# Optimization experiments

Hardware: AMD Instinct MI355X
Metric: run time of the kernel (lower is better)

## Reference

```python
import jax, jax.numpy as jnp
import numpy as np
import math

D_MODEL, N_HEADS, D_HEAD, D_MLP = 768, 12, 64, 3072
LN_EPS = 1e-5
INIT_STD = 0.02


def gelu_new(x):
    # GPT-2 'new' gelu: 0.5*x*(1+tanh(sqrt(2/pi)*(x+0.044715*x^3)))
    c = math.sqrt(2.0 / math.pi)
    return 0.5 * x * (1.0 + jnp.tanh(c * (x + 0.044715 * jnp.power(x, 3.0))))


def layer_norm(x, w, b):
    mu = jnp.mean(x, axis=-1, keepdims=True)
    xc = x - mu
    scale = jnp.sqrt(jnp.mean(xc * xc, axis=-1, keepdims=True) + LN_EPS)
    return (xc / scale) * w + b


def setup_inputs() -> dict:
    key = jax.random.key(0)
    ks = jax.random.split(key, 8)
    resid_pre = jax.random.normal(ks[0], (8, 1024, D_MODEL), dtype=jnp.float32)
    W_Q = jax.random.normal(ks[1], (N_HEADS, D_MODEL, D_HEAD), dtype=jnp.float32) * INIT_STD
    W_K = jax.random.normal(ks[2], (N_HEADS, D_MODEL, D_HEAD), dtype=jnp.float32) * INIT_STD
    W_V = jax.random.normal(ks[3], (N_HEADS, D_MODEL, D_HEAD), dtype=jnp.float32) * INIT_STD
    W_O = jax.random.normal(ks[4], (N_HEADS, D_HEAD, D_MODEL), dtype=jnp.float32) * INIT_STD
    W_in = jax.random.normal(ks[5], (D_MODEL, D_MLP), dtype=jnp.float32) * INIT_STD
    W_out = jax.random.normal(ks[6], (D_MLP, D_MODEL), dtype=jnp.float32) * INIT_STD
    return {
        'resid_pre': resid_pre,
        'ln1_w': jnp.ones((D_MODEL,), jnp.float32), 'ln1_b': jnp.zeros((D_MODEL,), jnp.float32),
        'W_Q': W_Q, 'b_Q': jnp.zeros((N_HEADS, D_HEAD), jnp.float32),
        'W_K': W_K, 'b_K': jnp.zeros((N_HEADS, D_HEAD), jnp.float32),
        'W_V': W_V, 'b_V': jnp.zeros((N_HEADS, D_HEAD), jnp.float32),
        'W_O': W_O, 'b_O': jnp.zeros((D_MODEL,), jnp.float32),
        'ln2_w': jnp.ones((D_MODEL,), jnp.float32), 'ln2_b': jnp.zeros((D_MODEL,), jnp.float32),
        'W_in': W_in, 'b_in': jnp.zeros((D_MLP,), jnp.float32),
        'W_out': W_out, 'b_out': jnp.zeros((D_MODEL,), jnp.float32),
    }


def attention(x, W_Q, b_Q, W_K, b_K, W_V, b_V, W_O, b_O):
    # x: [b, s, d_model]
    q = jnp.einsum('bsd,hde->bshe', x, W_Q) + b_Q
    k = jnp.einsum('bsd,hde->bshe', x, W_K) + b_K
    v = jnp.einsum('bsd,hde->bshe', x, W_V) + b_V
    scores = jnp.einsum('bqhe,bkhe->bhqk', q, k) / math.sqrt(D_HEAD)
    s = x.shape[1]
    causal = jnp.triu(jnp.ones((s, s), dtype=bool), k=1)
    scores = jnp.where(causal, -jnp.inf, scores)
    pattern = jax.nn.softmax(scores, axis=-1)
    pattern = jnp.where(jnp.isnan(pattern), 0.0, pattern)
    z = jnp.einsum('bhqk,bkhe->bqhe', pattern, v)
    # per-head projection then sum over heads; b_O/n_heads per head sums to b_O
    return jnp.einsum('bqhe,hed->bqd', z, W_O) + b_O


def reference(resid_pre, ln1_w, ln1_b, W_Q, b_Q, W_K, b_K, W_V, b_V, W_O, b_O,
              ln2_w, ln2_b, W_in, b_in, W_out, b_out):
    normed1 = layer_norm(resid_pre, ln1_w, ln1_b)
    attn_out = attention(normed1, W_Q, b_Q, W_K, b_K, W_V, b_V, W_O, b_O)
    residual = resid_pre + attn_out
    normed2 = layer_norm(residual, ln2_w, ln2_b)
    pre = jnp.einsum('bsd,dm->bsm', normed2, W_in) + b_in
    mlp_out = jnp.einsum('bsm,md->bsd', gelu_new(pre), W_out) + b_out
    return residual + mlp_out
```

## Files before the change

kernel.cpp:

```cpp
#include <hip/hip_runtime.h>
#include <hip/hip_bf16.h>
#include <stdint.h>
#include <math.h>

typedef __bf16 bf16x8 __attribute__((ext_vector_type(8)));
typedef float f32x4 __attribute__((ext_vector_type(4)));
using bf16 = __hip_bfloat16;

__device__ inline float bf2f(bf16 x) { return __bfloat162float(x); }
__device__ inline bf16 f2bf(float x) { return __float2bfloat16(x); }

__device__ inline f32x4 mfma16(bf16x8 a, bf16x8 b, f32x4 c) {
  return __builtin_amdgcn_mfma_f32_16x16x32_bf16(a, b, c, 0, 0, 0);
}

__device__ inline void async16(const bf16* g, bf16* l) {
  __builtin_amdgcn_global_load_lds(
      (const __attribute__((address_space(1))) unsigned int*)g,
      (__attribute__((address_space(3))) unsigned int*)l, 16, 0, 0);
}

__device__ inline float gelu_new(float x) {
  float u2 = 1.5957691216057308f * (x + 0.044715f * x * x * x);
  float e = __expf(u2);
  float t = 1.0f - 2.0f * __builtin_amdgcn_rcpf(e + 1.0f);
  return 0.5f * x * (1.0f + t);
}

__device__ inline void ln_body(const float* __restrict__ x, const float* __restrict__ w,
                               const float* __restrict__ bb, bf16* __restrict__ out,
                               int row, int t, float* red) {
  size_t base = (size_t)row * 768;
  float v0 = x[base + t];
  float v1 = x[base + t + 256];
  float v2 = x[base + t + 512];
  float s = v0 + v1 + v2;
  float ss = v0 * v0 + v1 * v1 + v2 * v2;
#pragma unroll
  for (int off = 32; off > 0; off >>= 1) {
    s += __shfl_down(s, off, 64);
    ss += __shfl_down(ss, off, 64);
  }
  int wv = t >> 6, ln = t & 63;
  if (ln == 0) { red[wv] = s; red[4 + wv] = ss; }
  __syncthreads();
  s = red[0] + red[1] + red[2] + red[3];
  ss = red[4] + red[5] + red[6] + red[7];
  float mu = s * (1.0f / 768.0f);
  float var = ss * (1.0f / 768.0f) - mu * mu;
  float rinv = rsqrtf(var + 1e-5f);
  out[base + t]       = f2bf((v0 - mu) * rinv * w[t]       + bb[t]);
  out[base + t + 256] = f2bf((v1 - mu) * rinv * w[t + 256] + bb[t + 256]);
  out[base + t + 512] = f2bf((v2 - mu) * rinv * w[t + 512] + bb[t + 512]);
}

__global__ __launch_bounds__(256) void ln_kernel(const float* __restrict__ x,
                                                 const float* __restrict__ w,
                                                 const float* __restrict__ bb,
                                                 bf16* __restrict__ out) {
  __shared__ float red[8];
  ln_body(x, w, bb, out, blockIdx.x, threadIdx.x, red);
}

__device__ inline void transpose_body(const float* __restrict__ in, bf16* __restrict__ out,
                                      int R, int C, int bx, int by, int t,
                                      float (*tile)[33]) {
  int tx = t & 31, ty = t >> 5;
  int r0 = bx * 32, c0 = by * 32;
#pragma unroll
  for (int j = 0; j < 32; j += 8)
    tile[ty + j][tx] = in[(size_t)(r0 + ty + j) * C + c0 + tx];
  __syncthreads();
#pragma unroll
  for (int j = 0; j < 32; j += 8)
    out[(size_t)(c0 + ty + j) * R + r0 + tx] = f2bf(tile[tx][ty + j]);
}

__global__ __launch_bounds__(256) void prep_all(
    const float* __restrict__ resid_pre, const float* __restrict__ ln1_w,
    const float* __restrict__ ln1_b, bf16* __restrict__ n1,
    const float* __restrict__ Wq, const float* __restrict__ Wk,
    const float* __restrict__ Wv, bf16* __restrict__ Wqkv_t,
    const float* __restrict__ W_O, bf16* __restrict__ Wo_t,
    const float* __restrict__ W_in, bf16* __restrict__ Win_t,
    const float* __restrict__ W_out, bf16* __restrict__ Wout_t,
    const float* __restrict__ bq, const float* __restrict__ bk,
    const float* __restrict__ bv, float* __restrict__ bias_qkv) {
  __shared__ float tile[32][33];
  const int t = threadIdx.x;
  int bid = blockIdx.x;
  if (bid < 8192) {
    ln_body(resid_pre, ln1_w, ln1_b, n1, bid, t, &tile[0][0]);
    return;
  }
  bid -= 8192;
  if (bid < 1728) {
    int z = bid / 48, r = bid - z * 48;
    int which = z / 12, h = z - which * 12;
    const float* W = (which == 0) ? Wq : ((which == 1) ? Wk : Wv);
    transpose_body(W + (size_t)h * 768 * 64,
                   Wqkv_t + (size_t)which * 589824 + (size_t)h * 64 * 768,
                   768, 64, r % 24, r / 24, t, tile);
    return;
  }
  bid -= 1728;
  if (bid < 576) {
    transpose_body(W_O, Wo_t, 768, 768, bid % 24, bid / 24, t, tile);
    return;
  }
  bid -= 576;
  if (bid < 2304) {
    transpose_body(W_in, Win_t, 768, 3072, bid % 24, bid / 24, t, tile);
    return;
  }
  bid -= 2304;
  if (bid < 2304) {
    transpose_body(W_out, Wout_t, 3072, 768, bid % 96, bid / 96, t, tile);
    return;
  }
  bid -= 2304;
  int i = bid * 256 + t;
  if (i < 2304)
    bias_qkv[i] = (i < 768) ? bq[i] : ((i < 1536) ? bk[i - 768] : bv[i - 1536]);
}

enum { MODE_QKV = 0, MODE_ADDF = 2, MODE_GELU = 3 };

template <int MODE, int MROWS>
__global__ __launch_bounds__(256) void gemm_bt(
    const bf16* __restrict__ A, const bf16* __restrict__ BT,
    const float* __restrict__ bias,
    const float* __restrict__ addend,
    float* __restrict__ out_f32,
    bf16* __restrict__ out_bf16,
    int M, int N, int K) {
  constexpr int MI = MROWS / 32;
  __shared__ __align__(16) bf16 smem[(MROWS + 128) * 64];
  bf16* Alds = smem;
  bf16* Blds = smem + MROWS * 64;
  const int t = threadIdx.x;
  const int wave = t >> 6, lane = t & 63;
  const int lm = lane & 15, quad = lane >> 4;
  const int wm = wave >> 1, wn = wave & 1;
  const int m0 = blockIdx.x * MROWS, n0 = blockIdx.y * 128;

  f32x4 acc[MI][4] = {};

  for (int k0 = 0; k0 < K; k0 += 64) {
#pragma unroll
    for (int i = 0; i < MI; i++) {
      int c = i * 256 + t;
      int r = c >> 3, cs = c & 7;
      async16(A + (size_t)(m0 + r) * K + k0 + ((cs ^ (r & 7)) << 3), &Alds[c * 8]);
    }
#pragma unroll
    for (int i = 0; i < 4; i++) {
      int c = i * 256 + t;
      int r = c >> 3, cs = c & 7;
      async16(BT + (size_t)(n0 + r) * K + k0 + ((cs ^ (r & 7)) << 3), &Blds[c * 8]);
    }
    __syncthreads();
#pragma unroll
    for (int kk = 0; kk < 64; kk += 32) {
      const int cbase = kk >> 3;
      bf16x8 af[MI], bfr[4];
#pragma unroll
      for (int mi = 0; mi < MI; mi++)
        af[mi] = *(const bf16x8*)&Alds[(wm * (MROWS / 2) + mi * 16 + lm) * 64 +
                                       (((cbase + quad) ^ (lm & 7)) << 3)];
#pragma unroll
      for (int ni = 0; ni < 4; ni++)
        bfr[ni] = *(const bf16x8*)&Blds[(wn * 64 + ni * 16 + lm) * 64 +
                                        (((cbase + quad) ^ (lm & 7)) << 3)];
#pragma unroll
      for (int mi = 0; mi < MI; mi++)
#pragma unroll
        for (int ni = 0; ni < 4; ni++)
          acc[mi][ni] = mfma16(af[mi], bfr[ni], acc[mi][ni]);
    }
    __syncthreads();
  }

  float bv[4];
#pragma unroll
  for (int ni = 0; ni < 4; ni++) bv[ni] = bias[n0 + wn * 64 + ni * 16 + lm];

  float* sc = (float*)smem + wave * 1088;
  const bool vseg = (MODE == MODE_QKV) && ((n0 + wn * 64) >= 1536);

#pragma unroll
  for (int mi = 0; mi < MI; mi++) {
    __syncthreads();
#pragma unroll
    for (int ni = 0; ni < 4; ni++)
#pragma unroll
      for (int reg = 0; reg < 4; reg++) {
        float val = acc[mi][ni][reg] + bv[ni];
        if (vseg) sc[(ni * 16 + lm) * 17 + quad * 4 + reg] = val;
        else      sc[(quad * 4 + reg) * 67 + ni * 16 + lm] = val;
      }
    __syncthreads();

    if (!vseg) {
#pragma unroll
      for (int p = 0; p < 2; p++) {
        int rl = p * 8 + (lane >> 3);
        int cl = (lane & 7) * 8;
        float v[8];
#pragma unroll
        for (int j = 0; j < 8; j++) v[j] = sc[rl * 67 + cl + j];
        int rm = m0 + wm * (MROWS / 2) + mi * 16 + rl;
        int cn0 = n0 + wn * 64 + cl;
        if constexpr (MODE == MODE_GELU) {
          bf16x8 o;
#pragma unroll
          for (int j = 0; j < 8; j++) o[j] = (__bf16)gelu_new(v[j]);
          *(bf16x8*)(out_bf16 + (size_t)rm * N + cn0) = o;
        } else if constexpr (MODE == MODE_ADDF) {
          size_t idx = (size_t)rm * N + cn0;
          f32x4 a0 = *(const f32x4*)(addend + idx);
          f32x4 a1 = *(const f32x4*)(addend + idx + 4);
          f32x4 o0, o1;
#pragma unroll
          for (int j = 0; j < 4; j++) { o0[j] = v[j] + a0[j]; o1[j] = v[4 + j] + a1[j]; }
          *(f32x4*)(out_f32 + idx) = o0;
          *(f32x4*)(out_f32 + idx + 4) = o1;
        } else {
          int seg = cn0 / 768;
          int lnn = cn0 - seg * 768;
          int h2 = lnn >> 6, e0 = lnn & 63;
          int b2 = rm >> 10, sq = rm & 1023;
          float scale = (seg == 0) ? 0.125f : 1.0f;
          bf16x8 o;
#pragma unroll
          for (int j = 0; j < 8; j++) o[j] = (__bf16)(v[j] * scale);
          *(bf16x8*)(out_bf16 + (size_t)seg * 6291456 +
                     (((size_t)(b2 * 12 + h2) * 1024 + sq) << 6) + e0) = o;
        }
      }
    } else {
#pragma unroll
      for (int p = 0; p < 2; p++) {
        float v[8];
#pragma unroll
        for (int j = 0; j < 8; j++) v[j] = sc[lane * 17 + p * 8 + j];
        int e_he = n0 + wn * 64 + lane;
        int lnn = e_he - 1536;
        int h2 = lnn >> 6, e2 = lnn & 63;
        int s0 = m0 + wm * (MROWS / 2) + mi * 16 + p * 8;
        int b2 = s0 >> 10, sq = s0 & 1023;
        bf16x8 o;
#pragma unroll
        for (int j = 0; j < 8; j++) o[j] = (__bf16)v[j];
        *(bf16x8*)(out_bf16 + (size_t)2 * 6291456 +
                   (((size_t)(b2 * 12 + h2) * 64 + e2) << 10) + sq) = o;
      }
    }
  }
}

__global__ __launch_bounds__(256) void attn_kernel(const bf16* __restrict__ q,
                                                   const bf16* __restrict__ k,
                                                   const bf16* __restrict__ vt,
                                                   bf16* __restrict__ z) {
  const int S = 1024, E = 64;
  __shared__ __align__(16) bf16 Klds[64 * 64];
  __shared__ __align__(16) bf16 Vlds[64 * 64];
  __shared__ __align__(16) bf16 Plds[4 * 16 * 64];
  const int pb = blockIdx.x;
  const int bh = blockIdx.y;
  const int t = threadIdx.x;
  const int wave = t >> 6, lane = t & 63;
  const int lm = lane & 15, quad = lane >> 4;
  const size_t bh_se = (size_t)bh * S * E;
  const int b = bh / 12, h = bh - b * 12;

  for (int seg = 0; seg < 2; seg++) {
    const int qt = seg ? (15 - pb) : pb;
    const int qrow = qt * 64 + wave * 16 + lm;
    bf16x8 qf0 = *(const bf16x8*)(q + bh_se + (size_t)qrow * E + quad * 8);
    bf16x8 qf1 = *(const bf16x8*)(q + bh_se + (size_t)qrow * E + 32 + quad * 8);

    f32x4 acco[4] = {};
    float lsum[4] = {0.f, 0.f, 0.f, 0.f};

    for (int kt = 0; kt <= qt; kt++) {
#pragma unroll
      for (int i = 0; i < 2; i++) {
        int c = i * 256 + t;
        int r = c >> 3, cs = c & 7;
        int sw = (cs ^ (r & 7)) << 3;
        async16(k + bh_se + (size_t)(kt * 64 + r) * E + sw, &Klds[c * 8]);
        async16(vt + bh_se + (size_t)r * S + kt * 64 + sw, &Vlds[c * 8]);
      }
      __syncthreads();

      f32x4 accs[4] = {};
#pragma unroll
      for (int ni = 0; ni < 4; ni++) {
        int row = ni * 16 + lm;
        bf16x8 kf0 = *(const bf16x8*)&Klds[row * 64 + ((quad ^ (lm & 7)) << 3)];
        bf16x8 kf1 = *(const bf16x8*)&Klds[row * 64 + (((4 + quad) ^ (lm & 7)) << 3)];
        accs[ni] = mfma16(qf0, kf0, accs[ni]);
        accs[ni] = mfma16(qf1, kf1, accs[ni]);
      }

      float pv[4][4];
      const int qg = wave * 16 + quad * 4;
      if (kt == qt) {
#pragma unroll
        for (int ni = 0; ni < 4; ni++)
#pragma unroll
          for (int reg = 0; reg < 4; reg++) {
            float e_ = __expf(accs[ni][reg]);
            pv[ni][reg] = ((ni * 16 + lm) > (qg + reg)) ? 0.f : e_;
          }
      } else {
#pragma unroll
        for (int ni = 0; ni < 4; ni++)
#pragma unroll
          for (int reg = 0; reg < 4; reg++)
            pv[ni][reg] = __expf(accs[ni][reg]);
      }

#pragma unroll
      for (int ni = 0; ni < 4; ni++)
#pragma unroll
        for (int reg = 0; reg < 4; reg++) {
          lsum[reg] += pv[ni][reg];
          int pr = quad * 4 + reg;
          int ce = ni * 16 + lm;
          Plds[wave * 1024 + pr * 64 + (((ce >> 3) ^ (pr & 7)) << 3) + (ce & 7)] =
              f2bf(pv[ni][reg]);
        }
      __syncthreads();

      bf16x8 pf0 = *(const bf16x8*)&Plds[wave * 1024 + lm * 64 + ((quad ^ (lm & 7)) << 3)];
      bf16x8 pf1 = *(const bf16x8*)&Plds[wave * 1024 + lm * 64 + (((4 + quad) ^ (lm & 7)) << 3)];
#pragma unroll
      for (int ni = 0; ni < 4; ni++) {
        int row = ni * 16 + lm;
        bf16x8 vf0 = *(const bf16x8*)&Vlds[row * 64 + ((quad ^ (lm & 7)) << 3)];
        bf16x8 vf1 = *(const bf16x8*)&Vlds[row * 64 + (((4 + quad) ^ (lm & 7)) << 3)];
        acco[ni] = mfma16(pf0, vf0, acco[ni]);
        acco[ni] = mfma16(pf1, vf1, acco[ni]);
      }
      __syncthreads();
    }

#pragma unroll
    for (int reg = 0; reg < 4; reg++) {
#pragma unroll
      for (int off = 1; off < 16; off <<= 1) lsum[reg] += __shfl_xor(lsum[reg], off, 16);
    }
    float rl[4];
#pragma unroll
    for (int reg = 0; reg < 4; reg++) rl[reg] = 1.0f / lsum[reg];

#pragma unroll
    for (int ni = 0; ni < 4; ni++)
#pragma unroll
      for (int reg = 0; reg < 4; reg++) {
        int srow = qt * 64 + wave * 16 + quad * 4 + reg;
        size_t idx = (((size_t)(b * 1024 + srow) * 12 + h) << 6) + ni * 16 + lm;
        z[idx] = f2bf(acco[ni][reg] * rl[reg]);
      }
  }
}

extern "C" void kernel_launch(void* const* d_in, const int* in_sizes, int n_in,
                              void* d_out, int out_size, void* d_ws, size_t ws_size,
                              hipStream_t stream) {
  (void)in_sizes; (void)n_in; (void)out_size; (void)ws_size;
  const float* resid_pre = (const float*)d_in[0];
  const float* ln1_w = (const float*)d_in[1];
  const float* ln1_b = (const float*)d_in[2];
  const float* W_Q = (const float*)d_in[3];
  const float* b_Q = (const float*)d_in[4];
  const float* W_K = (const float*)d_in[5];
  const float* b_K = (const float*)d_in[6];
  const float* W_V = (const float*)d_in[7];
  const float* b_V = (const float*)d_in[8];
  const float* W_O = (const float*)d_in[9];
  const float* b_O = (const float*)d_in[10];
  const float* ln2_w = (const float*)d_in[11];
  const float* ln2_b = (const float*)d_in[12];
  const float* W_in = (const float*)d_in[13];
  const float* b_in = (const float*)d_in[14];
  const float* W_out = (const float*)d_in[15];
  const float* b_out = (const float*)d_in[16];

  char* ws = (char*)d_ws;
  const size_t EB = (size_t)8192 * 768;
  bf16* n1     = (bf16*)(ws);
  bf16* qb     = (bf16*)(ws + EB * 2);
  bf16* zb     = (bf16*)(ws + EB * 8);
  float* resid = (float*)(ws + EB * 10);
  bf16* act    = (bf16*)(ws + EB * 2);
  char* wsw = ws + EB * 14;
  bf16* Wqkv_t = (bf16*)(wsw);
  bf16* Wo_t   = (bf16*)(wsw + 3 * 1179648);
  bf16* Win_t  = (bf16*)(wsw + 4 * 1179648);
  bf16* Wout_t = (bf16*)(wsw + 4 * 1179648 + 4718592);
  float* bias_qkv = (float*)(wsw + 4 * 1179648 + 4718592 + 9437184);
  bf16* kb  = qb + EB;
  bf16* vtb = qb + 2 * EB;

  prep_all<<<15113, 256, 0, stream>>>(resid_pre, ln1_w, ln1_b, n1,
                                      W_Q, W_K, W_V, Wqkv_t,
                                      W_O, Wo_t, W_in, Win_t, W_out, Wout_t,
                                      b_Q, b_K, b_V, bias_qkv);

  gemm_bt<MODE_QKV, 128><<<dim3(64, 18), 256, 0, stream>>>(
      n1, Wqkv_t, bias_qkv, nullptr, nullptr, qb, 8192, 2304, 768);

  attn_kernel<<<dim3(8, 96), 256, 0, stream>>>(qb, kb, vtb, zb);

  gemm_bt<MODE_ADDF, 64><<<dim3(128, 6), 256, 0, stream>>>(
      zb, Wo_t, b_O, resid_pre, resid, nullptr, 8192, 768, 768);

  ln_kernel<<<8192, 256, 0, stream>>>(resid, ln2_w, ln2_b, n1);

  gemm_bt<MODE_GELU, 128><<<dim3(64, 24), 256, 0, stream>>>(
      n1, Win_t, b_in, nullptr, nullptr, act, 8192, 3072, 768);
  gemm_bt<MODE_ADDF, 64><<<dim3(128, 6), 256, 0, stream>>>(
      act, Wout_t, b_out, resid, (float*)d_out, nullptr, 8192, 768, 3072);
}
```

Measured before the change: 340.0 us.

## Add 256x256-tile 8-wave pipelined GEMM for QKV and MLP-in projections

Introduces a new gemm256 kernel with 256x256 output tiles, 512 threads, a double-buffered LDS pipeline fed by async global-to-LDS loads, and four phases per k-step that interleave staging with MFMA work under s_setprio. It also adds an XCD-aware block swizzle. The kernel replaces the 128-tile gemm_bt for the QKV projection and the GELU MLP-in projection, aiming for more data reuse per tile and better overlap of loads with compute. It hardcodes K=768 and M=8192 and uses 128KB of LDS, which limits occupancy.

```diff
diff --git a/kernel.cpp b/kernel.cpp
--- a/kernel.cpp
+++ b/kernel.cpp
@@ -254,6 +254,203 @@
         for (int j = 0; j < 8; j++) o[j] = (__bf16)v[j];
         *(bf16x8*)(out_bf16 + (size_t)2 * 6291456 +
                    (((size_t)(b2 * 12 + h2) * 64 + e2) << 10) + sq) = o;
+      }
+    }
+  }
+}
+
+#define PHASE(BT_, AH, BH, STAGE, TAIL) do {                                          \
+  bf16x8 af_[4][2], bf_[2][2];                                                        \
+  _Pragma("unroll")                                                                   \
+  for (int f_ = 0; f_ < 4; f_++) {                                                    \
+    _Pragma("unroll")                                                                 \
+    for (int k_ = 0; k_ < 2; k_++)                                                    \
+      af_[f_][k_] = *(const bf16x8*)&sm[(BT_) * 32768 + (AH) * 8192 +                 \
+                                        (aRow + f_ * 16) * 64 +                       \
+                                        (((k_ * 4 + quad) ^ lms) << 3)];              \
+  }                                                                                   \
+  _Pragma("unroll")                                                                   \
+  for (int g_ = 0; g_ < 2; g_++) {                                                    \
+    _Pragma("unroll")                                                                 \
+    for (int k_ = 0; k_ < 2; k_++)                                                    \
+      bf_[g_][k_] = *(const bf16x8*)&sm[(BT_) * 32768 + 16384 + (BH) * 8192 +         \
+                                        (bRow + g_ * 16) * 64 +                       \
+                                        (((k_ * 4 + quad) ^ lms) << 3)];              \
+  }                                                                                   \
+  STAGE;                                                                              \
+  __builtin_amdgcn_s_barrier();                                                       \
+  __builtin_amdgcn_s_setprio(1);                                                      \
+  _Pragma("unroll")                                                                   \
+  for (int k_ = 0; k_ < 2; k_++) {                                                    \
+    _Pragma("unroll")                                                                 \
+    for (int f_ = 0; f_ < 4; f_++) {                                                  \
+      _Pragma("unroll")                                                               \
+      for (int g_ = 0; g_ < 2; g_++)                                                  \
+        acc[AH][f_][BH][g_] = mfma16(af_[f_][k_], bf_[g_][k_], acc[AH][f_][BH][g_]);  \
+    }                                                                                 \
+  }                                                                                   \
+  __builtin_amdgcn_s_setprio(0);                                                      \
+  TAIL;                                                                               \
+  __builtin_amdgcn_s_barrier();                                                       \
+} while (0)
+
+template <int MODE>
+__global__ __launch_bounds__(512, 2) void gemm256(
+    const bf16* __restrict__ A, const bf16* __restrict__ BT,
+    const float* __restrict__ bias, bf16* __restrict__ out, int N) {
+  __shared__ __align__(16) bf16 sm[65536];
+  const int tid = threadIdx.x;
+  const int wave = tid >> 6, lane = tid & 63;
+  const int lm = lane & 15, quad = lane >> 4, lms = lm & 7;
+  const int wm = wave >> 2, wn = wave & 3;
+
+  const int cpx = gridDim.x >> 3;
+  const int swz = (blockIdx.x & 7) * cpx + (blockIdx.x >> 3);
+  const int m0 = (swz & 31) * 256;
+  const int n0 = (swz >> 5) * 256;
+
+  const int aRow = wm * 64 + lm;
+  const int bRow = wn * 32 + lm;
+
+  const int r0 = tid >> 3;
+  const int of0 = (((tid & 7) ^ (r0 & 7)) << 3);
+  const bf16* sA = A + (size_t)(m0 + r0) * 768 + of0;
+  const bf16* sB = BT + (size_t)(n0 + r0) * 768 + of0;
+
+  auto STA = [&](int bb, int ah, int t2) {
+    bf16* d = sm + bb * 32768 + ah * 8192 + tid * 8;
+    const bf16* s = sA + ah * 98304 + t2 * 64;
+    async16(s, d);
+    async16(s + 49152, d + 4096);
+  };
+  auto STB = [&](int bb, int bh, int t2) {
+    bf16* d = sm + bb * 32768 + 16384 + bh * 8192 + tid * 8;
+    const bf16* s = sB + bh * 98304 + t2 * 64;
+    async16(s, d);
+    async16(s + 49152, d + 4096);
+  };
+
+  f32x4 acc[2][4][2][2] = {};
+
+  STA(0, 0, 0); STB(0, 0, 0); STA(0, 1, 0); STB(0, 1, 0);
+  STA(1, 0, 1); STB(1, 0, 1);
+  asm volatile("s_waitcnt vmcnt(4)" ::: "memory");
+  __builtin_amdgcn_s_barrier();
+
+#pragma unroll 2
+  for (int tt = 0; tt < 12; ++tt) {
+    const int bt = tt & 1;
+    PHASE(bt, 0, 0, { if (tt + 1 < 12) STA(bt ^ 1, 1, tt + 1); }, {});
+    PHASE(bt, 0, 1, { if (tt + 1 < 12) STB(bt ^ 1, 1, tt + 1); }, {});
+    PHASE(bt, 1, 0, { if (tt + 2 < 12) STA(bt, 0, tt + 2); }, {});
+    PHASE(bt, 1, 1, { if (tt + 2 < 12) STB(bt, 0, tt + 2); },
+          {
+            if (tt + 1 < 12) {
+              if (tt + 2 < 12) asm volatile("s_waitcnt vmcnt(4)" ::: "memory");
+              else             asm volatile("s_waitcnt vmcnt(0)" ::: "memory");
+            }
+          });
+  }
+
+  float bvv[2][2];
+#pragma unroll
+  for (int bh2 = 0; bh2 < 2; bh2++)
+#pragma unroll
+    for (int g = 0; g < 2; g++)
+      bvv[bh2][g] = bias[n0 + bh2 * 128 + wn * 32 + g * 16 + lm];
+
+  float* sc = (float*)sm + wave * 1088;
+
+  if constexpr (MODE == MODE_GELU) {
+#pragma unroll
+    for (int mi = 0; mi < 8; mi++) {
+      const int ah = mi >> 2, f = mi & 3;
+#pragma unroll
+      for (int bh2 = 0; bh2 < 2; bh2++)
+#pragma unroll
+        for (int g = 0; g < 2; g++)
+#pragma unroll
+          for (int reg = 0; reg < 4; reg++)
+            sc[(quad * 4 + reg) * 68 + bh2 * 32 + g * 16 + lm] =
+                acc[ah][f][bh2][g][reg] + bvv[bh2][g];
+#pragma unroll
+      for (int p = 0; p < 2; p++) {
+        int slot = p * 64 + lane;
+        int rw = slot >> 3, c8 = (slot & 7) * 8;
+        f32x4 u0 = *(const f32x4*)&sc[rw * 68 + c8];
+        f32x4 u1 = *(const f32x4*)&sc[rw * 68 + c8 + 4];
+        int grow = m0 + ah * 128 + wm * 64 + f * 16 + rw;
+        int bh3 = c8 >> 5, cc = c8 & 31;
+        int gcol = n0 + bh3 * 128 + wn * 32 + cc;
+        bf16x8 o;
+#pragma unroll
+        for (int j = 0; j < 4; j++) { o[j] = (__bf16)gelu_new(u0[j]); o[4 + j] = (__bf16)gelu_new(u1[j]); }
+        *(bf16x8*)(out + (size_t)grow * N + gcol) = o;
+      }
+    }
+  } else {
+    const int seg = n0 / 768;
+    const float scale = (seg == 0) ? 0.125f : 1.0f;
+    if (seg < 2) {
+      bf16* qout = out + (size_t)seg * 6291456;
+#pragma unroll
+      for (int mi = 0; mi < 8; mi++) {
+        const int ah = mi >> 2, f = mi & 3;
+#pragma unroll
+        for (int bh2 = 0; bh2 < 2; bh2++)
+#pragma unroll
+          for (int g = 0; g < 2; g++)
+#pragma unroll
+            for (int reg = 0; reg < 4; reg++)
+              sc[(quad * 4 + reg) * 68 + bh2 * 32 + g * 16 + lm] =
+                  (acc[ah][f][bh2][g][reg] + bvv[bh2][g]) * scale;
+#pragma unroll
+        for (int p = 0; p < 2; p++) {
+          int slot = p * 64 + lane;
+          int rw = slot >> 3, c8 = (slot & 7) * 8;
+          f32x4 u0 = *(const f32x4*)&sc[rw * 68 + c8];
+          f32x4 u1 = *(const f32x4*)&sc[rw * 68 + c8 + 4];
+          int grow = m0 + ah * 128 + wm * 64 + f * 16 + rw;
+          int bh3 = c8 >> 5, cc = c8 & 31;
+          int gcol = n0 + bh3 * 128 + wn * 32 + cc;
+          int lnn = gcol - seg * 768;
+          int h2 = lnn >> 6, e0 = lnn & 63;
+          int b2 = grow >> 10, sq = grow & 1023;
+          bf16x8 o;
+#pragma unroll
+          for (int j = 0; j < 4; j++) { o[j] = (__bf16)u0[j]; o[4 + j] = (__bf16)u1[j]; }
+          *(bf16x8*)(qout + (((size_t)(b2 * 12 + h2) * 1024 + sq) << 6) + e0) = o;
+        }
+      }
+    } else {
+#pragma unroll
+      for (int mi = 0; mi < 8; mi++) {
+        const int ah = mi >> 2, f = mi & 3;
+#pragma unroll
+        for (int bh2 = 0; bh2 < 2; bh2++)
+#pragma unroll
+          for (int g = 0; g < 2; g++)
+#pragma unroll
+            for (int reg = 0; reg < 4; reg++)
+              sc[(bh2 * 32 + g * 16 + lm) * 17 + quad * 4 + reg] =
+                  acc[ah][f][bh2][g][reg] + bvv[bh2][g];
+#pragma unroll
+        for (int p = 0; p < 2; p++) {
+          float v[8];
+#pragma unroll
+          for (int j = 0; j < 8; j++) v[j] = sc[lane * 17 + p * 8 + j];
+          int bh3 = lane >> 5, cc = lane & 31;
+          int gcol = n0 + bh3 * 128 + wn * 32 + cc;
+          int lnn = gcol - 1536;
+          int h2 = lnn >> 6, e2 = lnn & 63;
+          int s0 = m0 + ah * 128 + wm * 64 + f * 16 + p * 8;
+          int b2 = s0 >> 10, sq = s0 & 1023;
+          bf16x8 o;
+#pragma unroll
+          for (int j = 0; j < 8; j++) o[j] = (__bf16)v[j];
+          *(bf16x8*)(out + (size_t)2 * 6291456 +
+                     (((size_t)(b2 * 12 + h2) * 64 + e2) << 10) + sq) = o;
+        }
       }
     }
   }
@@ -411,8 +608,7 @@
                                       W_O, Wo_t, W_in, Win_t, W_out, Wout_t,
                                       b_Q, b_K, b_V, bias_qkv);
 
-  gemm_bt<MODE_QKV, 128><<<dim3(64, 18), 256, 0, stream>>>(
-      n1, Wqkv_t, bias_qkv, nullptr, nullptr, qb, 8192, 2304, 768);
+  gemm256<MODE_QKV><<<288, 512, 0, stream>>>(n1, Wqkv_t, bias_qkv, qb, 2304);
 
   attn_kernel<<<dim3(8, 96), 256, 0, stream>>>(qb, kb, vtb, zb);
 
@@ -421,8 +617,8 @@
 
   ln_kernel<<<8192, 256, 0, stream>>>(resid, ln2_w, ln2_b, n1);
 
-  gemm_bt<MODE_GELU, 128><<<dim3(64, 24), 256, 0, stream>>>(
-      n1, Win_t, b_in, nullptr, nullptr, act, 8192, 3072, 768);
+  gemm256<MODE_GELU><<<384, 512, 0, stream>>>(n1, Win_t, b_in, act, 3072);
+
   gemm_bt<MODE_ADDF, 64><<<dim3(128, 6), 256, 0, stream>>>(
       act, Wout_t, b_out, resid, (float*)d_out, nullptr, 8192, 768, 3072);
 }
```

New measurement: 364.5 us. 7.2% more time.
